# Performance work log

Hardware: AMD Instinct MI355X
Metric: run time of the kernel (lower is better)

The kernel has to match this reference:

```python
import jax, jax.numpy as jnp
import numpy as np

B, C, H, W = 4, 256, 128, 256
CQK = C // 4   # 64
COUT = 256


def setup_inputs() -> dict:
    key = jax.random.key(0)
    ks = jax.random.split(key, 8)
    s = 0.05
    return {
        "flow": jax.random.normal(ks[0], (B, C, H, W), jnp.float32),
        "de_out": jax.random.normal(ks[1], (B, C, H, W), jnp.float32),
        "Wq": jax.random.normal(ks[2], (CQK, C), jnp.float32) * s,
        "bq": jax.random.normal(ks[3], (CQK,), jnp.float32) * s,
        "Wk": jax.random.normal(ks[4], (CQK, C), jnp.float32) * s,
        "bk": jax.random.normal(ks[5], (CQK,), jnp.float32) * s,
        "Wv": jax.random.normal(ks[6], (COUT, C), jnp.float32) * s,
        "bv": jax.random.normal(ks[7], (COUT,), jnp.float32) * s,
    }


def reference(flow, de_out, Wq, bq, Wk, bk, Wv, bv):
    # 1x1 convs == channel-mixing einsums
    q = jnp.einsum('bchw,dc->bdhw', de_out, Wq) + bq[None, :, None, None]  # [B,CQK,H,W]
    k = jnp.einsum('bchw,dc->bdhw', flow, Wk) + bk[None, :, None, None]   # [B,CQK,H,W]
    v = jnp.einsum('bchw,oc->bohw', flow, Wv) + bv[None, :, None, None]   # [B,COUT,H,W]
    # width-axial attention: energy[b,h,w,w'] = sum_d q[b,d,h,w]*k[b,d,h,w']
    energy = jnp.einsum('bdhw,bdhv->bhwv', q, k)          # [B,H,W,W]
    att = jax.nn.softmax(energy, axis=-1)                 # softmax over key width w'
    # out[b,o,h,w] = sum_{w'} v[b,o,h,w'] * att[b,h,w,w']
    out = jnp.einsum('bohv,bhwv->bohw', v, att)           # [B,COUT,H,W]
    return out
```

## Files before the change

kernel.cpp:

```cpp
#include <hip/hip_runtime.h>

#define Bn   4
#define Cc   256
#define Hh   128
#define Ww   256
#define HWp  32768
#define CQK  64
#define COUT 256

typedef _Float16 half8 __attribute__((ext_vector_type(8)));
typedef _Float16 half4 __attribute__((ext_vector_type(4)));
typedef float   floatx4 __attribute__((ext_vector_type(4)));

#define MFMA16(a, b, c) __builtin_amdgcn_mfma_f32_16x16x32_f16((a), (b), (c), 0, 0, 0)

__global__ __launch_bounds__(256) void k_wcvt(
    const float* __restrict__ Wq, const float* __restrict__ Wk,
    const float* __restrict__ Wv, _Float16* __restrict__ W16f)
{
    const int g    = blockIdx.x * 256 + threadIdx.x;
    const int mt16 = g >> 9;
    const int ks   = (g >> 6) & 7;
    const int lane = g & 63;
    const int quad = lane >> 4;
    const int l16  = lane & 15;
    const int R    = mt16 * 16 + l16;
    const int c0   = ks * 32 + quad * 8;
    const float* src;
    if (R < 64)       src = Wq + (size_t)R * 256 + c0;
    else if (R < 128) src = Wk + (size_t)(R - 64) * 256 + c0;
    else              src = Wv + (size_t)(R - 128) * 256 + c0;
    float4 f0 = *(const float4*)src;
    float4 f1 = *(const float4*)(src + 4);
    half8 h = {(_Float16)f0.x, (_Float16)f0.y, (_Float16)f0.z, (_Float16)f0.w,
               (_Float16)f1.x, (_Float16)f1.y, (_Float16)f1.z, (_Float16)f1.w};
    *(half8*)&W16f[(size_t)g * 8] = h;
}

__device__ __forceinline__ int xswz(int row) { return ((row ^ (row >> 2)) & 7) << 3; }

__global__ __launch_bounds__(256, 4) void k_qkv(
    const float* __restrict__ flow, const float* __restrict__ de_out,
    const _Float16* __restrict__ W16f,
    const float* __restrict__ bq, const float* __restrict__ bk,
    const float* __restrict__ bv,
    _Float16* __restrict__ Qws, _Float16* __restrict__ Kws,
    _Float16* __restrict__ Vws)
{
    __shared__ __align__(16) _Float16 x_lds[64 * 256];

    const int t   = threadIdx.x;
    const int b   = blockIdx.y;
    const int job = blockIdx.z;
    const int pb  = blockIdx.x * 64;

    const float* X = (job == 0 ? de_out : flow) + (size_t)b * Cc * HWp;

    {
        const int px4 = t & 15;
        const int cg  = t >> 4;
        #pragma unroll
        for (int rep = 0; rep < 4; ++rep) {
            const int c0 = 4 * cg + 64 * rep;
            float4 r0 = *(const float4*)&X[(size_t)(c0 + 0) * HWp + pb + 4 * px4];
            float4 r1 = *(const float4*)&X[(size_t)(c0 + 1) * HWp + pb + 4 * px4];
            float4 r2 = *(const float4*)&X[(size_t)(c0 + 2) * HWp + pb + 4 * px4];
            float4 r3 = *(const float4*)&X[(size_t)(c0 + 3) * HWp + pb + 4 * px4];
            const int r = 4 * px4;
            half4 h;
            h = (half4){(_Float16)r0.x, (_Float16)r1.x, (_Float16)r2.x, (_Float16)r3.x};
            *(half4*)&x_lds[(r + 0) * 256 + (c0 ^ xswz(r + 0))] = h;
            h = (half4){(_Float16)r0.y, (_Float16)r1.y, (_Float16)r2.y, (_Float16)r3.y};
            *(half4*)&x_lds[(r + 1) * 256 + (c0 ^ xswz(r + 1))] = h;
            h = (half4){(_Float16)r0.z, (_Float16)r1.z, (_Float16)r2.z, (_Float16)r3.z};
            *(half4*)&x_lds[(r + 2) * 256 + (c0 ^ xswz(r + 2))] = h;
            h = (half4){(_Float16)r0.w, (_Float16)r1.w, (_Float16)r2.w, (_Float16)r3.w};
            *(half4*)&x_lds[(r + 3) * 256 + (c0 ^ xswz(r + 3))] = h;
        }
    }
    __syncthreads();

    const int wv   = t >> 6;
    const int lane = t & 63;
    const int quad = lane >> 4;
    const int l16  = lane & 15;
    const int n0   = (wv >> 1) * 32;
    const int wlo  = wv & 1;
    const int nmt  = (job == 0) ? 2 : 10;

    const int rowb0 = n0 + l16;
    const int rowb1 = n0 + 16 + l16;
    const int sw0 = xswz(rowb0);
    const int sw1 = xswz(rowb1);

    auto tile16 = [&](int mt) -> int {
        if (job == 0)  return mt * 2 + wlo;
        if (mt < 2)    return 4 + mt * 2 + wlo;
        return 8 + (mt - 2) * 2 + wlo;
    };

    const _Float16* apbase = W16f + (size_t)lane * 8;

    half8 a[8];
    {
        const size_t o0 = (size_t)tile16(0) * 4096;
        #pragma unroll
        for (int ks = 0; ks < 8; ++ks)
            a[ks] = *(const half8*)(apbase + o0 + ks * 512);
    }

    #pragma unroll 1
    for (int mt = 0; mt < nmt; ++mt) {
        half8 an[8];
        {
            const int mtn = (mt + 1 < nmt) ? mt + 1 : mt;
            const size_t on = (size_t)tile16(mtn) * 4096;
            #pragma unroll
            for (int ks = 0; ks < 8; ++ks)
                an[ks] = *(const half8*)(apbase + on + ks * 512);
        }

        floatx4 acc0 = {0.f, 0.f, 0.f, 0.f};
        floatx4 acc1 = {0.f, 0.f, 0.f, 0.f};
        #pragma unroll
        for (int ks = 0; ks < 8; ++ks) {
            half8 b0 = *(const half8*)&x_lds[rowb0 * 256 + ((ks * 32 + quad * 8) ^ sw0)];
            half8 b1 = *(const half8*)&x_lds[rowb1 * 256 + ((ks * 32 + quad * 8) ^ sw1)];
            acc0 = MFMA16(a[ks], b0, acc0);
            acc1 = MFMA16(a[ks], b1, acc1);
        }

        int mbase, dstmode;
        const float* bsel;
        _Float16* dst;
        if (job == 0)     { mbase = mt * 32;       bsel = bq; dst = Qws; dstmode = 0; }
        else if (mt < 2)  { mbase = mt * 32;       bsel = bk; dst = Kws; dstmode = 0; }
        else              { mbase = (mt - 2) * 32; bsel = bv; dst = Vws; dstmode = 1; }

        const int mloc = 16 * wlo + quad * 4;
        float4 bi = *(const float4*)&bsel[mbase + mloc];
        const float bia[4] = {bi.x, bi.y, bi.z, bi.w};
        if (dstmode == 0) {
            #pragma unroll
            for (int nt = 0; nt < 2; ++nt) {
                floatx4 acc = nt ? acc1 : acc0;
                const int pix = pb + n0 + nt * 16 + l16;
                half4 h = (half4){(_Float16)(acc[0] + bia[0]), (_Float16)(acc[1] + bia[1]),
                                  (_Float16)(acc[2] + bia[2]), (_Float16)(acc[3] + bia[3])};
                *(half4*)&dst[((size_t)b * HWp + pix) * 64 + mbase + mloc] = h;
            }
        } else {
            #pragma unroll
            for (int nt = 0; nt < 2; ++nt) {
                floatx4 acc = nt ? acc1 : acc0;
                const int pix = pb + n0 + nt * 16 + l16;
                #pragma unroll
                for (int r = 0; r < 4; ++r) {
                    const int o = mbase + mloc + r;
                    dst[((size_t)b * 256 + o) * HWp + pix] = (_Float16)(acc[r] + bia[r]);
                }
            }
        }

        #pragma unroll
        for (int ks = 0; ks < 8; ++ks) a[ks] = an[ks];
    }
}

__global__ __launch_bounds__(256, 2) void k_attn(
    const _Float16* __restrict__ Qws, const _Float16* __restrict__ Kws,
    const _Float16* __restrict__ Vws, float* __restrict__ out)
{
    __shared__ __align__(16) _Float16 k_lds[256 * 64];
    __shared__ __align__(16) _Float16 att_lds[32 * 256];
    __shared__ float inv_l[32];

    const int t    = threadIdx.x;
    const int h    = blockIdx.x;
    const int b    = blockIdx.y;
    const int wv   = t >> 6;
    const int lane = t & 63;
    const int quad = lane >> 4;
    const int l16  = lane & 15;
    const size_t pixbase = (size_t)b * HWp + h * 256;

    half8 vf[4][8];
    #pragma unroll
    for (int os = 0; os < 4; ++os)
        #pragma unroll
        for (int ks = 0; ks < 8; ++ks)
            vf[os][ks] = *(const half8*)&Vws[((size_t)b * 256 + os * 64 + 16 * wv + l16) * HWp
                                             + h * 256 + ks * 32 + quad * 8];

    #pragma unroll
    for (int i = 0; i < 8; ++i) {
        const int g = t + 256 * i;
        const int row = g >> 3, off = (g & 7) * 8;
        *(half8*)&k_lds[row * 64 + (off ^ ((row & 7) << 3))] =
            *(const half8*)&Kws[(pixbase + row) * 64 + off];
    }
    __syncthreads();

    const int wt  = wv & 1;
    const int swq = (l16 & 7) << 3;

    for (int chunk = 0; chunk < 8; ++chunk) {
        if (chunk) __syncthreads();

        {
            const size_t qrow = pixbase + chunk * 32 + wt * 16 + l16;
            half8 bq0 = *(const half8*)&Qws[qrow * 64 + quad * 8];
            half8 bq1 = *(const half8*)&Qws[qrow * 64 + 32 + quad * 8];
            #pragma unroll
            for (int j = 0; j < 8; ++j) {
                const int nt = (wv >> 1) * 8 + j;
                const int krow = nt * 16 + l16;
                half8 a0 = *(const half8*)&k_lds[krow * 64 + ((quad * 8) ^ swq)];
                half8 a1 = *(const half8*)&k_lds[krow * 64 + ((32 + quad * 8) ^ swq)];
                floatx4 acc = {0.f, 0.f, 0.f, 0.f};
                acc = MFMA16(a0, bq0, acc);
                acc = MFMA16(a1, bq1, acc);
                half4 hv = (half4){(_Float16)acc[0], (_Float16)acc[1],
                                   (_Float16)acc[2], (_Float16)acc[3]};
                *(half4*)&att_lds[(wt * 16 + l16) * 256 + ((nt * 16 + quad * 4) ^ swq)] = hv;
            }
        }
        __syncthreads();

        {
            const int r = t >> 3, seg = t & 7;
            const int sw = (r & 7) << 3;
            _Float16* base = &att_lds[r * 256];
            half8 v[4];
            float mx = -1e30f;
            #pragma unroll
            for (int u = 0; u < 4; ++u) {
                v[u] = *(const half8*)&base[(seg * 32 + u * 8) ^ sw];
                #pragma unroll
                for (int e = 0; e < 8; ++e) mx = fmaxf(mx, (float)v[u][e]);
            }
            mx = fmaxf(mx, __shfl_xor(mx, 1));
            mx = fmaxf(mx, __shfl_xor(mx, 2));
            mx = fmaxf(mx, __shfl_xor(mx, 4));
            float s = 0.f;
            #pragma unroll
            for (int u = 0; u < 4; ++u) {
                half8 ex;
                #pragma unroll
                for (int e = 0; e < 8; ++e) {
                    const float p = __expf((float)v[u][e] - mx);
                    s += p;
                    ex[e] = (_Float16)p;
                }
                *(half8*)&base[(seg * 32 + u * 8) ^ sw] = ex;
            }
            s += __shfl_xor(s, 1);
            s += __shfl_xor(s, 2);
            s += __shfl_xor(s, 4);
            if (seg == 0) inv_l[r] = 1.f / s;
        }
        __syncthreads();

        {
            floatx4 acc[4][2];
            #pragma unroll
            for (int os = 0; os < 4; ++os) {
                acc[os][0] = (floatx4){0.f, 0.f, 0.f, 0.f};
                acc[os][1] = (floatx4){0.f, 0.f, 0.f, 0.f};
            }
            #pragma unroll
            for (int ks = 0; ks < 8; ++ks) {
                half8 p0 = *(const half8*)&att_lds[l16 * 256 + ((ks * 32 + quad * 8) ^ swq)];
                half8 p1 = *(const half8*)&att_lds[(16 + l16) * 256 + ((ks * 32 + quad * 8) ^ swq)];
                #pragma unroll
                for (int os = 0; os < 4; ++os) {
                    acc[os][0] = MFMA16(vf[os][ks], p0, acc[os][0]);
                    acc[os][1] = MFMA16(vf[os][ks], p1, acc[os][1]);
                }
            }
            const float il0 = inv_l[l16];
            const float il1 = inv_l[16 + l16];
            const int wg = chunk * 32 + l16;
            #pragma unroll
            for (int os = 0; os < 4; ++os) {
                const int og = os * 64 + 16 * wv + quad * 4;
                #pragma unroll
                for (int r = 0; r < 4; ++r) {
                    out[(((size_t)b * 256 + og + r) * Hh + h) * Ww + wg]      = acc[os][0][r] * il0;
                    out[(((size_t)b * 256 + og + r) * Hh + h) * Ww + 16 + wg] = acc[os][1][r] * il1;
                }
            }
        }
    }
}

extern "C" void kernel_launch(void* const* d_in, const int* in_sizes, int n_in,
                              void* d_out, int out_size, void* d_ws, size_t ws_size,
                              hipStream_t stream)
{
    const float* flow   = (const float*)d_in[0];
    const float* de_out = (const float*)d_in[1];
    const float* Wq = (const float*)d_in[2];
    const float* bq = (const float*)d_in[3];
    const float* Wk = (const float*)d_in[4];
    const float* bk = (const float*)d_in[5];
    const float* Wv = (const float*)d_in[6];
    const float* bv = (const float*)d_in[7];

    _Float16* Qws = (_Float16*)d_ws;
    _Float16* Kws = Qws + (size_t)Bn * HWp * 64;
    _Float16* Vws = Kws + (size_t)Bn * HWp * 64;
    float* out = (float*)d_out;

    _Float16* W16f = (_Float16*)((char*)d_out + (size_t)out_size - 98304 * sizeof(_Float16));

    k_wcvt<<<dim3(48), 256, 0, stream>>>(Wq, Wk, Wv, W16f);

    dim3 g1(HWp / 64, Bn, 2);
    k_qkv<<<g1, 256, 0, stream>>>(flow, de_out, W16f, bq, bk, bv, Qws, Kws, Vws);

    dim3 g2(Hh, Bn);
    k_attn<<<g2, 256, 0, stream>>>(Qws, Kws, Vws, out);
}
```

Measured before the change: 400.1 us.

## Halve QKV projection pixel tile and raise occupancy, drop A-fragment prefetch

The QKV projection kernel now stages 32 pixels per block instead of 64, halving its LDS footprint and doubling the grid. Launch bounds go from 4 to 8 blocks per CU. Each wave now owns a distinct 16-row output slice across all 32 pixels, so the per-wave loop runs 1 or 5 steps instead of 2 or 10, and the register double-buffered weight prefetch is removed. The aim is more latency hiding through occupancy, at the cost of reloading the weights from global memory twice as often overall and losing the explicit weight prefetch.

```diff
diff --git a/kernel.cpp b/kernel.cpp
--- a/kernel.cpp
+++ b/kernel.cpp
@@ -39,7 +39,7 @@
 
 __device__ __forceinline__ int xswz(int row) { return ((row ^ (row >> 2)) & 7) << 3; }
 
-__global__ __launch_bounds__(256, 4) void k_qkv(
+__global__ __launch_bounds__(256, 8) void k_qkv(
     const float* __restrict__ flow, const float* __restrict__ de_out,
     const _Float16* __restrict__ W16f,
     const float* __restrict__ bq, const float* __restrict__ bk,
@@ -47,21 +47,21 @@
     _Float16* __restrict__ Qws, _Float16* __restrict__ Kws,
     _Float16* __restrict__ Vws)
 {
-    __shared__ __align__(16) _Float16 x_lds[64 * 256];
+    __shared__ __align__(16) _Float16 x_lds[32 * 256];
 
     const int t   = threadIdx.x;
     const int b   = blockIdx.y;
     const int job = blockIdx.z;
-    const int pb  = blockIdx.x * 64;
+    const int pb  = blockIdx.x * 32;
 
     const float* X = (job == 0 ? de_out : flow) + (size_t)b * Cc * HWp;
 
     {
-        const int px4 = t & 15;
-        const int cg  = t >> 4;
-        #pragma unroll
-        for (int rep = 0; rep < 4; ++rep) {
-            const int c0 = 4 * cg + 64 * rep;
+        const int px4 = t & 7;
+        const int cg  = t >> 3;
+        #pragma unroll
+        for (int rep = 0; rep < 2; ++rep) {
+            const int c0 = 4 * cg + 128 * rep;
             float4 r0 = *(const float4*)&X[(size_t)(c0 + 0) * HWp + pb + 4 * px4];
             float4 r1 = *(const float4*)&X[(size_t)(c0 + 1) * HWp + pb + 4 * px4];
             float4 r2 = *(const float4*)&X[(size_t)(c0 + 2) * HWp + pb + 4 * px4];
@@ -84,76 +84,53 @@
     const int lane = t & 63;
     const int quad = lane >> 4;
     const int l16  = lane & 15;
-    const int n0   = (wv >> 1) * 32;
-    const int wlo  = wv & 1;
-    const int nmt  = (job == 0) ? 2 : 10;
-
-    const int rowb0 = n0 + l16;
-    const int rowb1 = n0 + 16 + l16;
-    const int sw0 = xswz(rowb0);
-    const int sw1 = xswz(rowb1);
-
-    auto tile16 = [&](int mt) -> int {
-        if (job == 0)  return mt * 2 + wlo;
-        if (mt < 2)    return 4 + mt * 2 + wlo;
-        return 8 + (mt - 2) * 2 + wlo;
-    };
-
-    const _Float16* apbase = W16f + (size_t)lane * 8;
-
-    half8 a[8];
-    {
-        const size_t o0 = (size_t)tile16(0) * 4096;
+    const int nsteps = (job == 0) ? 1 : 5;
+
+    const int sw0 = xswz(l16);
+    const int sw1 = xswz(16 + l16);
+    const int mloc = wv * 16 + quad * 4;
+
+    #pragma unroll 1
+    for (int st = 0; st < nsteps; ++st) {
+        int tile16, mbase, dstmode;
+        const float* bsel;
+        _Float16* dst;
+        if (job == 0)     { tile16 = wv;                  mbase = 0;             bsel = bq; dst = Qws; dstmode = 0; }
+        else if (st == 0) { tile16 = 4 + wv;              mbase = 0;             bsel = bk; dst = Kws; dstmode = 0; }
+        else              { tile16 = 8 + (st - 1) * 4 + wv; mbase = (st - 1) * 64; bsel = bv; dst = Vws; dstmode = 1; }
+
+        half8 a[8];
+        const _Float16* ap = W16f + (size_t)tile16 * 4096 + (size_t)lane * 8;
         #pragma unroll
         for (int ks = 0; ks < 8; ++ks)
-            a[ks] = *(const half8*)(apbase + o0 + ks * 512);
-    }
-
-    #pragma unroll 1
-    for (int mt = 0; mt < nmt; ++mt) {
-        half8 an[8];
-        {
-            const int mtn = (mt + 1 < nmt) ? mt + 1 : mt;
-            const size_t on = (size_t)tile16(mtn) * 4096;
-            #pragma unroll
-            for (int ks = 0; ks < 8; ++ks)
-                an[ks] = *(const half8*)(apbase + on + ks * 512);
-        }
+            a[ks] = *(const half8*)(ap + ks * 512);
 
         floatx4 acc0 = {0.f, 0.f, 0.f, 0.f};
         floatx4 acc1 = {0.f, 0.f, 0.f, 0.f};
         #pragma unroll
         for (int ks = 0; ks < 8; ++ks) {
-            half8 b0 = *(const half8*)&x_lds[rowb0 * 256 + ((ks * 32 + quad * 8) ^ sw0)];
-            half8 b1 = *(const half8*)&x_lds[rowb1 * 256 + ((ks * 32 + quad * 8) ^ sw1)];
+            half8 b0 = *(const half8*)&x_lds[l16 * 256 + ((ks * 32 + quad * 8) ^ sw0)];
+            half8 b1 = *(const half8*)&x_lds[(16 + l16) * 256 + ((ks * 32 + quad * 8) ^ sw1)];
             acc0 = MFMA16(a[ks], b0, acc0);
             acc1 = MFMA16(a[ks], b1, acc1);
         }
 
-        int mbase, dstmode;
-        const float* bsel;
-        _Float16* dst;
-        if (job == 0)     { mbase = mt * 32;       bsel = bq; dst = Qws; dstmode = 0; }
-        else if (mt < 2)  { mbase = mt * 32;       bsel = bk; dst = Kws; dstmode = 0; }
-        else              { mbase = (mt - 2) * 32; bsel = bv; dst = Vws; dstmode = 1; }
-
-        const int mloc = 16 * wlo + quad * 4;
         float4 bi = *(const float4*)&bsel[mbase + mloc];
         const float bia[4] = {bi.x, bi.y, bi.z, bi.w};
         if (dstmode == 0) {
             #pragma unroll
             for (int nt = 0; nt < 2; ++nt) {
                 floatx4 acc = nt ? acc1 : acc0;
-                const int pix = pb + n0 + nt * 16 + l16;
+                const int pix = pb + nt * 16 + l16;
                 half4 h = (half4){(_Float16)(acc[0] + bia[0]), (_Float16)(acc[1] + bia[1]),
                                   (_Float16)(acc[2] + bia[2]), (_Float16)(acc[3] + bia[3])};
-                *(half4*)&dst[((size_t)b * HWp + pix) * 64 + mbase + mloc] = h;
+                *(half4*)&dst[((size_t)b * HWp + pix) * 64 + mloc] = h;
             }
         } else {
             #pragma unroll
             for (int nt = 0; nt < 2; ++nt) {
                 floatx4 acc = nt ? acc1 : acc0;
-                const int pix = pb + n0 + nt * 16 + l16;
+                const int pix = pb + nt * 16 + l16;
                 #pragma unroll
                 for (int r = 0; r < 4; ++r) {
                     const int o = mbase + mloc + r;
@@ -161,9 +138,6 @@
                 }
             }
         }
-
-        #pragma unroll
-        for (int ks = 0; ks < 8; ++ks) a[ks] = an[ks];
     }
 }
 
@@ -316,7 +290,7 @@
 
     k_wcvt<<<dim3(48), 256, 0, stream>>>(Wq, Wk, Wv, W16f);
 
-    dim3 g1(HWp / 64, Bn, 2);
+    dim3 g1(HWp / 32, Bn, 2);
     k_qkv<<<g1, 256, 0, stream>>>(flow, de_out, W16f, bq, bk, bv, Qws, Kws, Vws);
 
     dim3 g2(Hh, Bn);
```

Result: slower. 568.1 us (+42.0%).
